# Kernel tuning notes

Hardware: AMD Instinct MI355X
Metric: run time of the kernel (lower is better)

Reference implementation:

```python
import jax, jax.numpy as jnp
import numpy as np

N = 4096
DIN = 512
H = 128    # hidden_dim per head
K = 4      # num_heads
DOUT = 16  # output classes
ALPHA = 0.2  # leaky relu negative slope


def setup_inputs() -> dict:
    key = jax.random.key(0)
    ks = jax.random.split(key, 8)
    X = jax.random.normal(ks[0], (N, DIN), jnp.float32)
    # sparse random graph (p=0.01), non-zero where edges exist
    adj = (jax.random.uniform(ks[1], (N, N)) < 0.01).astype(jnp.float32)
    W1 = jax.random.normal(ks[2], (K, DIN, H), jnp.float32) * np.float32(1.0 / np.sqrt(DIN))
    a_src1 = jax.random.normal(ks[3], (K, H), jnp.float32) * np.float32(0.1)
    a_dst1 = jax.random.normal(ks[4], (K, H), jnp.float32) * np.float32(0.1)
    W2 = jax.random.normal(ks[5], (K * H, DOUT), jnp.float32) * np.float32(1.0 / np.sqrt(K * H))
    a_src2 = jax.random.normal(ks[6], (DOUT,), jnp.float32) * np.float32(0.1)
    a_dst2 = jax.random.normal(ks[7], (DOUT,), jnp.float32) * np.float32(0.1)
    return {"X": X, "adj": adj, "W1": W1, "a_src1": a_src1, "a_dst1": a_dst1,
            "W2": W2, "a_src2": a_src2, "a_dst2": a_dst2}


def gat_multihead(h, mask, W, a_src, a_dst):
    # h: (N, Din), W: (K, Din, O), a_src/a_dst: (K, O), mask: (N, N) bool
    Wh = jnp.einsum('ni,kio->kno', h, W)                      # (K, N, O)
    src = jnp.einsum('kno,ko->kn', Wh, a_src)                 # (K, N)
    dst = jnp.einsum('kno,ko->kn', Wh, a_dst)                 # (K, N)
    e = jax.nn.leaky_relu(src[:, :, None] + dst[:, None, :], ALPHA)  # (K, N, N)
    e = jnp.where(mask[None], e, -jnp.inf)
    attn = jax.nn.softmax(e, axis=-1)                         # rows sum to 1 (self-loop guarantees >=1 edge)
    return jnp.einsum('knm,kmo->kno', attn, Wh)               # (K, N, O)


def reference(X, adj, W1, a_src1, a_dst1, W2, a_src2, a_dst2):
    # mask = (adj + I) > 0
    mask = (adj + jnp.eye(N, dtype=adj.dtype)) > 0
    # layer 1: 4 heads, concatenated, then ELU (eval mode: no dropout)
    h1 = gat_multihead(X, mask, W1, a_src1, a_dst1)           # (K, N, H)
    h1 = jnp.transpose(h1, (1, 0, 2)).reshape(N, K * H)       # concat heads -> (N, K*H)
    h1 = jax.nn.elu(h1)
    # layer 2: single head, mean over heads == the head itself
    h2 = gat_multihead(h1, mask, W2[None], a_src2[None], a_dst2[None])[0]  # (N, DOUT)
    return jax.nn.log_softmax(h2, axis=1)
```

## Files before the change

kernel.cpp:

```cpp
#include <hip/hip_runtime.h>
#include <hip/hip_bf16.h>


typedef __attribute__((ext_vector_type(4))) float floatx4;
typedef __attribute__((ext_vector_type(8))) short short8;
typedef __attribute__((ext_vector_type(4))) unsigned short ushortx4;
typedef unsigned short u16b;

#define GN 4096
#define LDP 40

__device__ __forceinline__ u16b f2bf(float f) {
  union { float f; unsigned int i; } v; v.f = f;
  unsigned int r = v.i + 0x7FFF + ((v.i >> 16) & 1);
  return (u16b)(r >> 16);
}
__device__ __forceinline__ float bflo(unsigned u) {
  union { unsigned i; float f; } v; v.i = u << 16; return v.f;
}
__device__ __forceinline__ float bfhi(unsigned u) {
  union { unsigned i; float f; } v; v.i = u & 0xffff0000u; return v.f;
}

__global__ __launch_bounds__(512) void k_fused1(const float* __restrict__ adj,
    const float* __restrict__ X, const float* __restrict__ W1,
    const float* __restrict__ as1, const float* __restrict__ ad1,
    u16b* __restrict__ mask, u16b* __restrict__ Wh1bf,
    float* __restrict__ src1t, float* __restrict__ dst1t) {
  int b = blockIdx.x, t = threadIdx.x;
  int lane = t & 63, w = t >> 6;
  if (b >= 256) {
    int n = (b - 256) * 2 + (t >> 8);
    int cg = t & 255;
    const float* ap = adj + (size_t)n * 4096 + cg * 16;
    floatx4 v0 = *(const floatx4*)(ap);
    floatx4 v1 = *(const floatx4*)(ap + 4);
    floatx4 v2 = *(const floatx4*)(ap + 8);
    floatx4 v3 = *(const floatx4*)(ap + 12);
    unsigned bits = 0;
#pragma unroll
    for (int i = 0; i < 4; ++i) {
      bits |= (unsigned)(v0[i] != 0.f) << i;
      bits |= (unsigned)(v1[i] != 0.f) << (4 + i);
      bits |= (unsigned)(v2[i] != 0.f) << (8 + i);
      bits |= (unsigned)(v3[i] != 0.f) << (12 + i);
    }
    if ((n >> 4) == cg) bits |= 1u << (n & 15);
    mask[(size_t)n * 256 + cg] = (u16b)bits;
  } else {
    __shared__ u16b Ab[64 * LDP];
    __shared__ u16b Bb[128 * LDP];
    __shared__ float sps[4][64], sds[4][64];
    int p = ((b >> 5) << 3) | (b & 7);
    int hd = (b >> 3) & 3;
    int rb = p * 64;
    const float* Wk = W1 + (size_t)hd * 65536;
    int wr = w >> 2, wc = w & 3, lh = lane >> 4, lm = lane & 15;
    int ar = t >> 2, aq = t & 3;
    int u = t - 256, kk0 = (u & 7) * 4, c0 = (u >> 3) * 4;
    floatx4 pa0, pa1, pb0, pb1, pb2, pb3;
    if (t < 256) {
      const float* ap = X + (size_t)(rb + ar) * 512 + aq * 8;
      pa0 = *(const floatx4*)(ap);
      pa1 = *(const floatx4*)(ap + 4);
    } else {
      const float* bp = Wk + (size_t)kk0 * 128 + c0;
      pb0 = *(const floatx4*)(bp);
      pb1 = *(const floatx4*)(bp + 128);
      pb2 = *(const floatx4*)(bp + 256);
      pb3 = *(const floatx4*)(bp + 384);
    }
    floatx4 acc[2][2] = {};
    for (int kk = 0; kk < 512; kk += 32) {
      if (t < 256) {
        short8 a;
        a[0] = (short)f2bf(pa0[0]); a[1] = (short)f2bf(pa0[1]);
        a[2] = (short)f2bf(pa0[2]); a[3] = (short)f2bf(pa0[3]);
        a[4] = (short)f2bf(pa1[0]); a[5] = (short)f2bf(pa1[1]);
        a[6] = (short)f2bf(pa1[2]); a[7] = (short)f2bf(pa1[3]);
        *(short8*)(&Ab[ar * LDP + aq * 8]) = a;
      } else {
#pragma unroll
        for (int cq = 0; cq < 4; ++cq) {
          ushortx4 v;
          v[0] = f2bf(pb0[cq]); v[1] = f2bf(pb1[cq]);
          v[2] = f2bf(pb2[cq]); v[3] = f2bf(pb3[cq]);
          *(ushortx4*)(&Bb[(c0 + cq) * LDP + kk0]) = v;
        }
      }
      __syncthreads();
      if (kk + 32 < 512) {
        if (t < 256) {
          const float* ap = X + (size_t)(rb + ar) * 512 + kk + 32 + aq * 8;
          pa0 = *(const floatx4*)(ap);
          pa1 = *(const floatx4*)(ap + 4);
        } else {
          const float* bp = Wk + (size_t)(kk + 32 + kk0) * 128 + c0;
          pb0 = *(const floatx4*)(bp);
          pb1 = *(const floatx4*)(bp + 128);
          pb2 = *(const floatx4*)(bp + 256);
          pb3 = *(const floatx4*)(bp + 384);
        }
      }
      short8 a0 = *(const short8*)(&Ab[(wr * 32      + lm) * LDP + lh * 8]);
      short8 a1 = *(const short8*)(&Ab[(wr * 32 + 16 + lm) * LDP + lh * 8]);
      short8 b0 = *(const short8*)(&Bb[(wc * 32      + lm) * LDP + lh * 8]);
      short8 b1 = *(const short8*)(&Bb[(wc * 32 + 16 + lm) * LDP + lh * 8]);
      acc[0][0] = __builtin_amdgcn_mfma_f32_16x16x32_bf16(a0, b0, acc[0][0], 0, 0, 0);
      acc[0][1] = __builtin_amdgcn_mfma_f32_16x16x32_bf16(a0, b1, acc[0][1], 0, 0, 0);
      acc[1][0] = __builtin_amdgcn_mfma_f32_16x16x32_bf16(a1, b0, acc[1][0], 0, 0, 0);
      acc[1][1] = __builtin_amdgcn_mfma_f32_16x16x32_bf16(a1, b1, acc[1][1], 0, 0, 0);
      __syncthreads();
    }
#pragma unroll
    for (int m = 0; m < 2; ++m)
#pragma unroll
      for (int n2 = 0; n2 < 2; ++n2)
#pragma unroll
        for (int j = 0; j < 4; ++j)
          Wh1bf[(size_t)(rb + wr * 32 + m * 16 + lh * 4 + j) * 512
                + hd * 128 + wc * 32 + n2 * 16 + lm] = f2bf(acc[m][n2][j]);
    float asv[2], adv[2];
#pragma unroll
    for (int n2 = 0; n2 < 2; ++n2) {
      asv[n2] = as1[hd * 128 + wc * 32 + n2 * 16 + lm];
      adv[n2] = ad1[hd * 128 + wc * 32 + n2 * 16 + lm];
    }
#pragma unroll
    for (int m = 0; m < 2; ++m)
#pragma unroll
      for (int j = 0; j < 4; ++j) {
        float ps = acc[m][0][j] * asv[0] + acc[m][1][j] * asv[1];
        float pd = acc[m][0][j] * adv[0] + acc[m][1][j] * adv[1];
#pragma unroll
        for (int off = 8; off >= 1; off >>= 1) {
          ps += __shfl_xor(ps, off, 16);
          pd += __shfl_xor(pd, off, 16);
        }
        if (lm == 0) {
          sps[wc][wr * 32 + m * 16 + lh * 4 + j] = ps;
          sds[wc][wr * 32 + m * 16 + lh * 4 + j] = pd;
        }
      }
    __syncthreads();
    if (t < 64) {
      src1t[(size_t)(rb + t) * 4 + hd] = sps[0][t] + sps[1][t] + sps[2][t] + sps[3][t];
      dst1t[(size_t)(rb + t) * 4 + hd] = sds[0][t] + sds[1][t] + sds[2][t] + sds[3][t];
    }
  }
}

__global__ __launch_bounds__(256) void k_attn1(const u16b* __restrict__ mask,
    const u16b* __restrict__ Wh1bf,
    const float* __restrict__ src1t, const float* __restrict__ dst1t,
    const float* __restrict__ W2, const float* __restrict__ as2,
    const float* __restrict__ ad2, float* __restrict__ Wh2,
    float* __restrict__ src2, float* __restrict__ dst2) {
  int n = blockIdx.x, t = threadIdx.x, lane = t & 63, w = t >> 6;
  __shared__ u16b lst[512];
  __shared__ float ew[4][516];
  __shared__ float h1row[512];
  __shared__ float redw[4][16];
  __shared__ int wtot[4];
  unsigned M = mask[(size_t)n * 256 + t];
  int pc = __popc(M);
  int incl = pc;
#pragma unroll
  for (int off = 1; off <= 32; off <<= 1) {
    int v = __shfl_up(incl, off);
    if (lane >= off) incl += v;
  }
  if (lane == 63) wtot[w] = incl;
  float sn[4];
#pragma unroll
  for (int k = 0; k < 4; ++k) sn[k] = src1t[n * 4 + k];
  __syncthreads();
  int base = 0;
  for (int w2 = 0; w2 < w; ++w2) base += wtot[w2];
  int cnt = wtot[0] + wtot[1] + wtot[2] + wtot[3];
  int pos = base + incl - pc;
  while (M) {
    int c = __builtin_ctz(M);
    lst[pos++] = (u16b)(t * 16 + c);
    M &= M - 1;
  }
  __syncthreads();
  for (int j = t; j < cnt * 4; j += 256) {
    int li = j >> 2, k = j & 3;
    int m = lst[li];
    float e = sn[k] + dst1t[m * 4 + k];
    ew[k][li] = e > 0.f ? e : 0.2f * e;
  }
  __syncthreads();
  {
    float mx = -1e30f, sm = 0.f;
    for (int li = lane; li < cnt; li += 64) {
      float e = ew[w][li];
      if (e > mx) { sm = sm * __expf(mx - e) + 1.f; mx = e; }
      else sm += __expf(e - mx);
    }
#pragma unroll
    for (int off = 32; off >= 1; off >>= 1) {
      float mo = __shfl_xor(mx, off);
      float so = __shfl_xor(sm, off);
      float Mx = fmaxf(mx, mo);
      sm = sm * __expf(mx - Mx) + so * __expf(mo - Mx);
      mx = Mx;
    }
    float R = 1.f / sm;
    for (int li = lane; li < cnt; li += 64)
      ew[w][li] = __expf(ew[w][li] - mx) * R;
  }
  __syncthreads();
  float a0 = 0.f, a1 = 0.f;
  const float* ewk = ew[w];
#pragma unroll 4
  for (int li = 0; li < cnt; ++li) {
    int m = lst[li];
    float wv = ewk[li];
    unsigned uu = *(const unsigned*)(Wh1bf + (size_t)m * 512 + 2 * t);
    a0 = fmaf(wv, bflo(uu), a0);
    a1 = fmaf(wv, bfhi(uu), a1);
  }
  a0 = a0 > 0.f ? a0 : __expf(a0) - 1.f;
  a1 = a1 > 0.f ? a1 : __expf(a1) - 1.f;
  h1row[2 * t] = a0;
  h1row[2 * t + 1] = a1;
  __syncthreads();
  {
    int o = lane & 15, ig = lane >> 4;
    float accw = 0.f;
    for (int i = w * 128 + ig; i < (w + 1) * 128; i += 4)
      accw = fmaf(h1row[i], W2[i * 16 + o], accw);
    accw += __shfl_xor(accw, 16);
    accw += __shfl_xor(accw, 32);
    if (lane < 16) redw[w][o] = accw;
  }
  __syncthreads();
  if (t < 16) {
    float v = redw[0][t] + redw[1][t] + redw[2][t] + redw[3][t];
    Wh2[n * 16 + t] = v;
    float ps = v * as2[t];
    float pd = v * ad2[t];
#pragma unroll
    for (int off = 8; off >= 1; off >>= 1) {
      ps += __shfl_xor(ps, off, 16);
      pd += __shfl_xor(pd, off, 16);
    }
    if (t == 0) { src2[n] = ps; dst2[n] = pd; }
  }
}

__global__ __launch_bounds__(256) void k_attn2(const u16b* __restrict__ mask,
    const float* __restrict__ Wh2, const float* __restrict__ src2,
    const float* __restrict__ dst2, float* __restrict__ out) {
  int w = threadIdx.x >> 6, lane = threadIdx.x & 63;
  int n = blockIdx.x * 4 + w;
  __shared__ u16b lst4[4][512];
  u16b* lst = lst4[w];
  unsigned long long B = *(const unsigned long long*)((const char*)mask + (size_t)n * 512 + lane * 8);
  int pc = __popcll(B);
  int incl = pc;
#pragma unroll
  for (int off = 1; off <= 32; off <<= 1) {
    int v = __shfl_up(incl, off);
    if (lane >= off) incl += v;
  }
  int cnt = __shfl(incl, 63);
  int pos = incl - pc;
  while (B) {
    int c = __builtin_ctzll(B);
    lst[pos++] = (u16b)(lane * 64 + c);
    B &= B - 1;
  }
  float snv = src2[n];
  float mx = -1e30f, sm = 0.f;
  for (int li = lane; li < cnt; li += 64) {
    int m = lst[li];
    float e = snv + dst2[m]; e = e > 0.f ? e : 0.2f * e;
    if (e > mx) { sm = sm * __expf(mx - e) + 1.f; mx = e; }
    else sm += __expf(e - mx);
  }
#pragma unroll
  for (int off = 32; off >= 1; off >>= 1) {
    float mo = __shfl_xor(mx, off);
    float so = __shfl_xor(sm, off);
    float M = fmaxf(mx, mo);
    sm = sm * __expf(mx - M) + so * __expf(mo - M);
    mx = M;
  }
  float R = 1.f / sm;
  int o = lane & 15, g = lane >> 4;
  float acc = 0.f;
  for (int li = g; li < cnt; li += 4) {
    int m = lst[li];
    float e = snv + dst2[m]; e = e > 0.f ? e : 0.2f * e;
    float wgt = __expf(e - mx) * R;
    acc = fmaf(wgt, Wh2[m * 16 + o], acc);
  }
  acc += __shfl_xor(acc, 16);
  acc += __shfl_xor(acc, 32);
  float vm = acc;
#pragma unroll
  for (int off = 8; off >= 1; off >>= 1) vm = fmaxf(vm, __shfl_xor(vm, off, 16));
  float ex = __expf(acc - vm);
#pragma unroll
  for (int off = 8; off >= 1; off >>= 1) ex += __shfl_xor(ex, off, 16);
  if (lane < 16) out[(size_t)n * 16 + lane] = acc - vm - __logf(ex);
}

extern "C" void kernel_launch(void* const* d_in, const int* in_sizes, int n_in,
                              void* d_out, int out_size, void* d_ws, size_t ws_size,
                              hipStream_t stream) {
  const float* X   = (const float*)d_in[0];
  const float* adj = (const float*)d_in[1];
  const float* W1  = (const float*)d_in[2];
  const float* as1 = (const float*)d_in[3];
  const float* ad1 = (const float*)d_in[4];
  const float* W2  = (const float*)d_in[5];
  const float* as2 = (const float*)d_in[6];
  const float* ad2 = (const float*)d_in[7];
  float* out = (float*)d_out;

  char* ws = (char*)d_ws;
  float* src1t = (float*)ws;
  float* dst1t = (float*)(ws + (64 << 10));
  float* src2  = (float*)(ws + (128 << 10));
  float* dst2  = (float*)(ws + (144 << 10));
  float* Wh2   = (float*)(ws + (160 << 10));
  u16b*  mask  = (u16b*)(ws + (512 << 10));
  u16b*  Wh1bf = (u16b*)(ws + (4ull << 20));

  k_fused1<<<dim3(2304), dim3(512), 0, stream>>>(adj, X, W1, as1, ad1,
                                                 mask, Wh1bf, src1t, dst1t);
  k_attn1<<<dim3(GN), dim3(256), 0, stream>>>(mask, Wh1bf, src1t, dst1t,
                                              W2, as2, ad2, Wh2, src2, dst2);
  k_attn2<<<dim3(1024), dim3(256), 0, stream>>>(mask, Wh2, src2, dst2, out);
}
```

Measured before the change: 67.00 us.

## Restructure layer-1 aggregation to per-head wave with 16-byte gathers and packed index/weight pairs

In the layer-1 attention kernel, each wave now handles one head. It computes its edge logits and online softmax in registers, then stores packed (row offset, weight) pairs to shared memory, which removes one block barrier and the separate logit pass. The weighted aggregation now has each lane load 16 bytes (8 bf16 values) per edge, with four edge groups combined by a cross-lane reduction, replacing 4-byte loads per lane. The layer-2 kernel fuses logit computation into list building and caches the logits so the second pass no longer re-gathers dst2. The trade-offs are higher register use (8 accumulators plus the cached arrays) and a fixed cap of 512 neighbors per row.

Result: no change. 67.45 us (+0.7%).

```diff
diff --git a/kernel.cpp b/kernel.cpp
--- a/kernel.cpp
+++ b/kernel.cpp
@@ -5,6 +5,7 @@
 typedef __attribute__((ext_vector_type(4))) float floatx4;
 typedef __attribute__((ext_vector_type(8))) short short8;
 typedef __attribute__((ext_vector_type(4))) unsigned short ushortx4;
+typedef __attribute__((ext_vector_type(4))) unsigned int uintx4;
 typedef unsigned short u16b;
 
 #define GN 4096
@@ -158,7 +159,7 @@
     float* __restrict__ src2, float* __restrict__ dst2) {
   int n = blockIdx.x, t = threadIdx.x, lane = t & 63, w = t >> 6;
   __shared__ u16b lst[512];
-  __shared__ float ew[4][516];
+  __shared__ int2 pr[4][512];
   __shared__ float h1row[512];
   __shared__ float redw[4][16];
   __shared__ int wtot[4];
@@ -171,9 +172,7 @@
     if (lane >= off) incl += v;
   }
   if (lane == 63) wtot[w] = incl;
-  float sn[4];
-#pragma unroll
-  for (int k = 0; k < 4; ++k) sn[k] = src1t[n * 4 + k];
+  float snw = src1t[n * 4 + w];
   __syncthreads();
   int base = 0;
   for (int w2 = 0; w2 < w; ++w2) base += wtot[w2];
@@ -185,47 +184,66 @@
     M &= M - 1;
   }
   __syncthreads();
-  for (int j = t; j < cnt * 4; j += 256) {
-    int li = j >> 2, k = j & 3;
-    int m = lst[li];
-    float e = sn[k] + dst1t[m * 4 + k];
-    ew[k][li] = e > 0.f ? e : 0.2f * e;
-  }
-  __syncthreads();
-  {
-    float mx = -1e30f, sm = 0.f;
-    for (int li = lane; li < cnt; li += 64) {
-      float e = ew[w][li];
+  float ee[8];
+  int mo[8];
+  float mx = -1e30f, sm = 0.f;
+#pragma unroll
+  for (int rep = 0; rep < 8; ++rep) {
+    int li = lane + rep * 64;
+    if (li < cnt) {
+      int m = lst[li];
+      float e = snw + dst1t[m * 4 + w];
+      e = e > 0.f ? e : 0.2f * e;
+      ee[rep] = e; mo[rep] = m << 10;
       if (e > mx) { sm = sm * __expf(mx - e) + 1.f; mx = e; }
       else sm += __expf(e - mx);
     }
-#pragma unroll
-    for (int off = 32; off >= 1; off >>= 1) {
-      float mo = __shfl_xor(mx, off);
-      float so = __shfl_xor(sm, off);
-      float Mx = fmaxf(mx, mo);
-      sm = sm * __expf(mx - Mx) + so * __expf(mo - Mx);
-      mx = Mx;
-    }
-    float R = 1.f / sm;
-    for (int li = lane; li < cnt; li += 64)
-      ew[w][li] = __expf(ew[w][li] - mx) * R;
-  }
-  __syncthreads();
-  float a0 = 0.f, a1 = 0.f;
-  const float* ewk = ew[w];
-#pragma unroll 4
-  for (int li = 0; li < cnt; ++li) {
-    int m = lst[li];
-    float wv = ewk[li];
-    unsigned uu = *(const unsigned*)(Wh1bf + (size_t)m * 512 + 2 * t);
-    a0 = fmaf(wv, bflo(uu), a0);
-    a1 = fmaf(wv, bfhi(uu), a1);
-  }
-  a0 = a0 > 0.f ? a0 : __expf(a0) - 1.f;
-  a1 = a1 > 0.f ? a1 : __expf(a1) - 1.f;
-  h1row[2 * t] = a0;
-  h1row[2 * t + 1] = a1;
+  }
+#pragma unroll
+  for (int off = 32; off >= 1; off >>= 1) {
+    float mm = __shfl_xor(mx, off);
+    float so = __shfl_xor(sm, off);
+    float Mx = fmaxf(mx, mm);
+    sm = sm * __expf(mx - Mx) + so * __expf(mm - Mx);
+    mx = Mx;
+  }
+  float R = 1.f / sm;
+#pragma unroll
+  for (int rep = 0; rep < 8; ++rep) {
+    int li = lane + rep * 64;
+    if (li < cnt) {
+      int2 pv;
+      pv.x = mo[rep];
+      pv.y = __float_as_int(__expf(ee[rep] - mx) * R);
+      pr[w][li] = pv;
+    }
+  }
+  __syncthreads();
+  int q = lane >> 4, p = lane & 15;
+  const char* gbase = (const char*)Wh1bf + 256 * w + 16 * p;
+  float a[8] = {0.f, 0.f, 0.f, 0.f, 0.f, 0.f, 0.f, 0.f};
+  for (int li = q; li < cnt; li += 4) {
+    int2 pw = pr[w][li];
+    float wv = __int_as_float(pw.y);
+    uintx4 u = *(const uintx4*)(gbase + pw.x);
+    a[0] = fmaf(wv, bflo(u[0]), a[0]); a[1] = fmaf(wv, bfhi(u[0]), a[1]);
+    a[2] = fmaf(wv, bflo(u[1]), a[2]); a[3] = fmaf(wv, bfhi(u[1]), a[3]);
+    a[4] = fmaf(wv, bflo(u[2]), a[4]); a[5] = fmaf(wv, bfhi(u[2]), a[5]);
+    a[6] = fmaf(wv, bflo(u[3]), a[6]); a[7] = fmaf(wv, bfhi(u[3]), a[7]);
+  }
+#pragma unroll
+  for (int j = 0; j < 8; ++j) {
+    a[j] += __shfl_xor(a[j], 16);
+    a[j] += __shfl_xor(a[j], 32);
+  }
+  if (q == 0) {
+#pragma unroll
+    for (int j = 0; j < 8; ++j) {
+      float v = a[j];
+      v = v > 0.f ? v : __expf(v) - 1.f;
+      h1row[128 * w + 8 * p + j] = v;
+    }
+  }
   __syncthreads();
   {
     int o = lane & 15, ig = lane >> 4;
@@ -256,8 +274,9 @@
     const float* __restrict__ dst2, float* __restrict__ out) {
   int w = threadIdx.x >> 6, lane = threadIdx.x & 63;
   int n = blockIdx.x * 4 + w;
-  __shared__ u16b lst4[4][512];
-  u16b* lst = lst4[w];
+  __shared__ int2 pr4[4][512];
+  int2* pr = pr4[w];
+  float snv = src2[n];
   unsigned long long B = *(const unsigned long long*)((const char*)mask + (size_t)n * 512 + lane * 8);
   int pc = __popcll(B);
   int incl = pc;
@@ -268,18 +287,17 @@
   }
   int cnt = __shfl(incl, 63);
   int pos = incl - pc;
+  float mx = -1e30f, sm = 0.f;
   while (B) {
     int c = __builtin_ctzll(B);
-    lst[pos++] = (u16b)(lane * 64 + c);
-    B &= B - 1;
-  }
-  float snv = src2[n];
-  float mx = -1e30f, sm = 0.f;
-  for (int li = lane; li < cnt; li += 64) {
-    int m = lst[li];
-    float e = snv + dst2[m]; e = e > 0.f ? e : 0.2f * e;
+    int m = lane * 64 + c;
+    float e = snv + dst2[m];
+    e = e > 0.f ? e : 0.2f * e;
     if (e > mx) { sm = sm * __expf(mx - e) + 1.f; mx = e; }
     else sm += __expf(e - mx);
+    int2 pv; pv.x = m << 4; pv.y = __float_as_int(e);
+    pr[pos++] = pv;
+    B &= B - 1;
   }
 #pragma unroll
   for (int off = 32; off >= 1; off >>= 1) {
@@ -293,10 +311,9 @@
   int o = lane & 15, g = lane >> 4;
   float acc = 0.f;
   for (int li = g; li < cnt; li += 4) {
-    int m = lst[li];
-    float e = snv + dst2[m]; e = e > 0.f ? e : 0.2f * e;
-    float wgt = __expf(e - mx) * R;
-    acc = fmaf(wgt, Wh2[m * 16 + o], acc);
+    int2 pv = pr[li];
+    float wgt = __expf(__int_as_float(pv.y) - mx) * R;
+    acc = fmaf(wgt, Wh2[pv.x + o], acc);
   }
   acc += __shfl_xor(acc, 16);
   acc += __shfl_xor(acc, 32);
```
